# Optimization experiments

Measured on AMD Instinct MI355X. Metric: run time of the kernel, lower is better.

## Reference

```python
import jax, jax.numpy as jnp
import numpy as np

D_MODEL = 128
NUM_HEADS = 8
DEPTH = D_MODEL // NUM_HEADS
NEG = -1e9


def _dense_params(key, d_in, d_out):
    kw, kb = jax.random.split(key)
    # Glorot-uniform like keras Dense default
    lim = np.sqrt(6.0 / (d_in + d_out))
    w = jax.random.uniform(kw, (d_in, d_out), jnp.float32, -lim, lim)
    b = jnp.zeros((d_out,), jnp.float32)
    return w, b


def setup_inputs() -> dict:
    key = jax.random.key(0)
    ks = jax.random.split(key, 16)
    B, N, M, d = 256, 128, 128, D_MODEL
    inp = {
        'x_self': jax.random.normal(ks[0], (B, N, d), jnp.float32),
        'adj_self': jax.random.randint(ks[1], (B, N, N), 0, 2, jnp.int32),
        'mask_self': jnp.ones((B, N), jnp.int32),
        'x_cross': jax.random.normal(ks[2], (B, M, d), jnp.float32),
        'mask_cross': jnp.ones((B, M), jnp.int32),
    }
    names = ['wq_s', 'wk_s', 'wv_s', 'wo_s', 'wq_c', 'wk_c', 'wv_c', 'wo_c']
    for i, nm in enumerate(names):
        w, b = _dense_params(ks[3 + i], d, d)
        inp[nm] = w
        inp['b' + nm[1:]] = b
    wg, bg = _dense_params(ks[12], 3 * d, d)
    inp['wg'] = wg
    inp['bg'] = bg
    return inp


def _split_heads(x):
    B, N, _ = x.shape
    return x.reshape(B, N, NUM_HEADS, DEPTH).transpose(0, 2, 1, 3)  # [B,H,N,depth]


def _merge_heads(x):
    B, H, N, Dp = x.shape
    return x.transpose(0, 2, 1, 3).reshape(B, N, H * Dp)


def _attention(q, k, v, mask, adj=None):
    # q,k,v: [B,H,Nq,depth]; mask: [B,Nk]; adj: [B,Nq,Nk] or None
    logits = jnp.einsum('bhqd,bhkd->bhqk', q, k) / jnp.sqrt(jnp.float32(DEPTH))
    if adj is not None:
        logits = logits + ((1.0 - adj.astype(jnp.float32)) * NEG)[:, None, :, :]
    logits = logits + ((1.0 - mask.astype(jnp.float32)) * NEG)[:, None, None, :]
    w = jax.nn.softmax(logits, axis=-1)
    return jnp.einsum('bhqk,bhkd->bhqd', w, v)


def reference(x_self, adj_self, mask_self, x_cross, mask_cross,
              wq_s, bq_s, wk_s, bk_s, wv_s, bv_s, wo_s, bo_s,
              wq_c, bq_c, wk_c, bk_c, wv_c, bv_c, wo_c, bo_c,
              wg, bg):
    # Self attention (adjacency + padding mask)
    q_s = _split_heads(x_self @ wq_s + bq_s)
    k_s = _split_heads(x_self @ wk_s + bk_s)
    v_s = _split_heads(x_self @ wv_s + bv_s)
    out_s = _merge_heads(_attention(q_s, k_s, v_s, mask_self, adj_self)) @ wo_s + bo_s
    # Cross attention (padding mask only); dropout inactive at inference
    q_c = _split_heads(x_self @ wq_c + bq_c)
    k_c = _split_heads(x_cross @ wk_c + bk_c)
    v_c = _split_heads(x_cross @ wv_c + bv_c)
    out_c = _merge_heads(_attention(q_c, k_c, v_c, mask_cross)) @ wo_c + bo_c
    # Sigmoid gate fusion
    gate = jax.nn.sigmoid(jnp.concatenate([x_self, out_s, out_c], axis=-1) @ wg + bg)
    return (1.0 - gate) * out_s + gate * out_c
```

## Files before the change

### kernel.cpp

```cpp
#include <hip/hip_runtime.h>
#include <hip/hip_bf16.h>

typedef _Float16 f16_t;
typedef __attribute__((ext_vector_type(8))) _Float16 f16x8;
typedef __attribute__((ext_vector_type(4))) float f32x4;

#define LFENCE() asm volatile("" ::: "memory")

__device__ __forceinline__ f16x8 cvt8(const float* p) {
  float4 v0 = *(const float4*)p;
  float4 v1 = *(const float4*)(p + 4);
  f16x8 a;
  a[0] = (f16_t)v0.x; a[1] = (f16_t)v0.y; a[2] = (f16_t)v0.z; a[3] = (f16_t)v0.w;
  a[4] = (f16_t)v1.x; a[5] = (f16_t)v1.y; a[6] = (f16_t)v1.z; a[7] = (f16_t)v1.w;
  return a;
}

__global__ __launch_bounds__(256) void prep_kernel(
    const float* wq_s, const float* wk_s, const float* wv_s,
    const float* wq_c, const float* wk_c, const float* wv_c,
    const float* wo_s, const float* wo_c, const float* wg,
    const float* bos, const float* boc, const float* bgin,
    f16_t* WT, float* bgp)
{
  const int b = blockIdx.x;
  const int tid = threadIdx.x;
  if (b < 11) {
    __shared__ float t[128][129];
    const float* src; f16_t* dst; int ostride;
    switch (b) {
      case 0: src = wq_s; break; case 1: src = wk_s; break;
      case 2: src = wv_s; break; case 3: src = wq_c; break;
      case 4: src = wk_c; break; case 5: src = wv_c; break;
      case 6: src = wo_s; break; case 7: src = wo_c; break;
      default: src = wg + (size_t)(b - 8) * 16384; break;
    }
    if (b < 8) { dst = WT + (size_t)b * 16384; ostride = 128; }
    else       { dst = WT + 8 * 16384 + (b - 8) * 128; ostride = 384; }
#pragma unroll
    for (int i = 0; i < 64; ++i) {
      const int idx = tid + i * 256;
      t[idx & 127][idx >> 7] = src[idx];
    }
    __syncthreads();
#pragma unroll
    for (int i = 0; i < 64; ++i) {
      const int idx = tid + i * 256;
      const int c = idx >> 7, r = idx & 127;
      dst[(size_t)c * ostride + r] = (f16_t)t[c][r];
    }
  } else if (b < 13) {
    const int matsel = b - 11;
    const float* wo = matsel ? wo_c : wo_s;
    const int joff = 128 + matsel * 128;
    f16_t* dst = WT + (size_t)(11 + matsel) * 16384;
    const int wv = tid >> 6, ln = tid & 63, l15 = ln & 15, g = ln >> 4;
    f32x4 acc[2][8];
#pragma unroll
    for (int mm = 0; mm < 2; ++mm)
#pragma unroll
      for (int nt = 0; nt < 8; ++nt) acc[mm][nt] = (f32x4){0.f, 0.f, 0.f, 0.f};
#pragma unroll
    for (int kt = 0; kt < 4; ++kt) {
      f16x8 a[2];
#pragma unroll
      for (int mm = 0; mm < 2; ++mm) {
        const int crow = wv * 32 + mm * 16 + l15;
#pragma unroll
        for (int jj = 0; jj < 8; ++jj)
          a[mm][jj] = (f16_t)wg[(size_t)(joff + kt * 32 + g * 8 + jj) * 128 + crow];
      }
#pragma unroll
      for (int nt = 0; nt < 8; ++nt) {
        f16x8 bf = cvt8(wo + (size_t)(nt * 16 + l15) * 128 + kt * 32 + g * 8);
        acc[0][nt] = __builtin_amdgcn_mfma_f32_16x16x32_f16(a[0], bf, acc[0][nt], 0, 0, 0);
        acc[1][nt] = __builtin_amdgcn_mfma_f32_16x16x32_f16(a[1], bf, acc[1][nt], 0, 0, 0);
      }
    }
#pragma unroll
    for (int mm = 0; mm < 2; ++mm)
#pragma unroll
      for (int nt = 0; nt < 8; ++nt)
#pragma unroll
        for (int r = 0; r < 4; ++r) {
          const int c = wv * 32 + mm * 16 + g * 4 + r;
          dst[(size_t)c * 128 + nt * 16 + l15] = (f16_t)acc[mm][nt][r];
        }
  } else {
    if (tid < 128) {
      float acc = bgin[tid];
      for (int j = 0; j < 128; ++j)
        acc += bos[j] * wg[(size_t)(128 + j) * 128 + tid] +
               boc[j] * wg[(size_t)(256 + j) * 128 + tid];
      bgp[tid] = acc;
    }
  }
}

template <bool TRANSP>
__device__ __forceinline__ void gemm8(
    const f16x8 afr[4], const f16_t* __restrict__ W, const float* __restrict__ bias,
    char* Ob, int l15, int g, int rg)
{
  f32x4 acc[8];
#pragma unroll
  for (int nt = 0; nt < 8; ++nt) acc[nt] = (f32x4){0.f, 0.f, 0.f, 0.f};
#pragma unroll
  for (int nt = 0; nt < 8; ++nt)
#pragma unroll
    for (int kt = 0; kt < 4; ++kt) {
      f16x8 b = *(const f16x8*)(W + (size_t)(nt * 16 + l15) * 128 + kt * 32 + g * 8);
      acc[nt] = __builtin_amdgcn_mfma_f32_16x16x32_f16(afr[kt], b, acc[nt], 0, 0, 0);
    }
#pragma unroll
  for (int nt = 0; nt < 8; ++nt) {
    const int col = nt * 16 + l15;
    const float bv = bias[col];
#pragma unroll
    for (int r = 0; r < 4; ++r) {
      const int row = rg * 16 + g * 4 + r;
      const f16_t v = (f16_t)(acc[nt][r] + bv);
      if (TRANSP)
        *(f16_t*)(Ob + col * 256 + ((row * 2) ^ ((col & 7) << 4))) = v;
      else
        *(f16_t*)(Ob + row * 256 + ((col * 2) ^ ((row & 7) << 4))) = v;
    }
  }
}

__device__ __forceinline__ void gemmQ2(
    const f16x8 afr[4], const f16_t* __restrict__ W, const float* __restrict__ bias,
    char* scr, int l15, int g, f16x8 bq[8])
{
#pragma unroll
  for (int p = 0; p < 2; ++p) {
    LFENCE();
    f32x4 acc[4];
#pragma unroll
    for (int nt = 0; nt < 4; ++nt) acc[nt] = (f32x4){0.f, 0.f, 0.f, 0.f};
#pragma unroll
    for (int nt = 0; nt < 4; ++nt)
#pragma unroll
      for (int kt = 0; kt < 4; ++kt) {
        f16x8 b = *(const f16x8*)(W + (size_t)(p * 64 + nt * 16 + l15) * 128 + kt * 32 + g * 8);
        acc[nt] = __builtin_amdgcn_mfma_f32_16x16x32_f16(afr[kt], b, acc[nt], 0, 0, 0);
      }
#pragma unroll
    for (int nt = 0; nt < 4; ++nt) {
      const float bv = bias[p * 64 + nt * 16 + l15];
      const int dloc = nt * 16 + l15;
#pragma unroll
      for (int r = 0; r < 4; ++r) {
        const int qp = g * 4 + r;
        *(f16_t*)(scr + qp * 128 + ((dloc * 2) ^ ((qp & 7) << 4))) = (f16_t)(acc[nt][r] + bv);
      }
    }
    LFENCE();
#pragma unroll
    for (int h = 0; h < 4; ++h) {
      f16x8 z = {0, 0, 0, 0, 0, 0, 0, 0};
      bq[p * 4 + h] = (g < 2)
        ? *(const f16x8*)(scr + l15 * 128 + (((h * 16 + g * 8) * 2) ^ ((l15 & 7) << 4)))
        : z;
    }
  }
  LFENCE();
}

__global__ __launch_bounds__(512) void battn_kernel(
    const float* __restrict__ Xs, const float* __restrict__ Xc,
    const int* __restrict__ adj, const int* __restrict__ mask_s,
    const int* __restrict__ mask_c, const f16_t* __restrict__ WT,
    const float* __restrict__ bq_s, const float* __restrict__ bk_s,
    const float* __restrict__ bv_s, const float* __restrict__ bq_c,
    const float* __restrict__ bk_c, const float* __restrict__ bv_c,
    f16_t* __restrict__ att_s, f16_t* __restrict__ att_c)
{
  __shared__ __align__(16) char Kb[32768];
  __shared__ __align__(16) char Vtb[32768];
  __shared__ __align__(16) char WS[16384];

  const bool self = blockIdx.x < 256;
  const int bb = blockIdx.x & 255;
  const int tid = threadIdx.x;
  const int rg = tid >> 6, ln = tid & 63, l15 = ln & 15, g = ln >> 4;
  const int arow = rg * 16 + l15;
  char* scr = WS + rg * 2048;

  const f16_t* WQ = WT + (size_t)(self ? 0 : 3) * 16384;
  const f16_t* WK = WT + (size_t)(self ? 1 : 4) * 16384;
  const f16_t* WV = WT + (size_t)(self ? 2 : 5) * 16384;
  const float* bqv = self ? bq_s : bq_c;
  const float* bkv = self ? bk_s : bk_c;
  const float* bvv = self ? bv_s : bv_c;
  const float* XK  = self ? Xs : Xc;
  const int* mask  = self ? mask_s : mask_c;
  f16_t* ATT = self ? att_s : att_c;

  unsigned mw[4];
  {
    unsigned long long m0 = __ballot(mask[bb * 128 + ln] != 0);
    unsigned long long m1 = __ballot(mask[bb * 128 + 64 + ln] != 0);
    mw[0] = (unsigned)m0; mw[1] = (unsigned)(m0 >> 32);
    mw[2] = (unsigned)m1; mw[3] = (unsigned)(m1 >> 32);
  }
  unsigned aw[4];
  if (self) {
    const int row = rg * 16 + (ln & 15);
    const int w = ln >> 4;
    const int4* ap = (const int4*)(adj + ((size_t)bb * 128 + row) * 128 + w * 32);
    unsigned word = 0;
#pragma unroll
    for (int i = 0; i < 8; ++i) {
      int4 a = ap[i];
      word |= ((a.x != 0 ? 1u : 0u) | (a.y != 0 ? 2u : 0u) |
               (a.z != 0 ? 4u : 0u) | (a.w != 0 ? 8u : 0u)) << (i * 4);
    }
#pragma unroll
    for (int w2 = 0; w2 < 4; ++w2)
      aw[w2] = (unsigned)__shfl((int)word, w2 * 16 + l15) & mw[w2];
  } else {
#pragma unroll
    for (int w2 = 0; w2 < 4; ++w2) aw[w2] = mw[w2];
  }

  f16x8 bq[8];
  {
    f16x8 afrK[4];
#pragma unroll
    for (int kt = 0; kt < 4; ++kt)
      afrK[kt] = cvt8(XK + (size_t)bb * 16384 + arow * 128 + kt * 32 + g * 8);
    gemm8<false>(afrK, WK, bkv, Kb, l15, g, rg);
    gemm8<true >(afrK, WV, bvv, Vtb, l15, g, rg);
    f16x8 afrQ[4];
    if (self) {
#pragma unroll
      for (int kt = 0; kt < 4; ++kt) afrQ[kt] = afrK[kt];
    } else {
#pragma unroll
      for (int kt = 0; kt < 4; ++kt)
        afrQ[kt] = cvt8(Xs + (size_t)bb * 16384 + arow * 128 + kt * 32 + g * 8);
    }
    gemmQ2(afrQ, WQ, bqv, scr, l15, g, bq);
  }
  __syncthreads();

  const f32x4 zero = (f32x4){0.f, 0.f, 0.f, 0.f};
  char* Pw = scr;
#pragma unroll
  for (int h = 0; h < 8; ++h) {
    const int d = h * 16 + l15;
    float psum = 0.f;
    f32x4 o = zero;
#pragma unroll
    for (int c = 0; c < 4; ++c) {
      f32x4 st[2];
#pragma unroll
      for (int hf = 0; hf < 2; ++hf) {
        const int krow = (c * 2 + hf) * 16 + l15;
        f16x8 ak = {0, 0, 0, 0, 0, 0, 0, 0};
        if (g < 2)
          ak = *(const f16x8*)(Kb + krow * 256 + (((h * 16 + g * 8) * 2) ^ ((krow & 7) << 4)));
        st[hf] = __builtin_amdgcn_mfma_f32_16x16x32_f16(ak, bq[h], zero, 0, 0, 0);
      }
#pragma unroll
      for (int hf = 0; hf < 2; ++hf) {
        union { f16_t hh[4]; unsigned long long u; } pk;
#pragma unroll
        for (int r = 0; r < 4; ++r) {
          const int k = (c * 2 + hf) * 16 + g * 4 + r;
          const float e = __expf(st[hf][r] * 0.25f - 4.f);
          const float p = ((aw[k >> 5] >> (k & 31)) & 1u) ? e : 0.f;
          psum += p;
          pk.hh[r] = (f16_t)p;
        }
        *(unsigned long long*)(Pw + l15 * 80 + hf * 32 + g * 8) = pk.u;
      }
      LFENCE();
      union { unsigned long long u[2]; f16x8 v; } pa2;
      pa2.u[0] = *(const unsigned long long*)(Pw + l15 * 80 + g * 16);
      pa2.u[1] = *(const unsigned long long*)(Pw + l15 * 80 + g * 16 + 8);
      LFENCE();
      f16x8 vb = *(const f16x8*)(Vtb + d * 256 + (((c * 32 + g * 8) * 2) ^ ((d & 7) << 4)));
      o = __builtin_amdgcn_mfma_f32_16x16x32_f16(pa2.v, vb, o, 0, 0, 0);
    }
    psum += __shfl_xor(psum, 16);
    psum += __shfl_xor(psum, 32);
    const float inv = 1.f / psum;
#pragma unroll
    for (int r = 0; r < 4; ++r) {
      const float invq = __shfl(inv, g * 4 + r);
      const int row = rg * 16 + g * 4 + r;
      ATT[(size_t)bb * 16384 + row * 128 + h * 16 + l15] = (f16_t)(o[r] * invq);
    }
  }
}

__global__ __launch_bounds__(256) void outgate2_kernel(
    const f16_t* __restrict__ AS, const f16_t* __restrict__ AC,
    const float* __restrict__ X, const f16_t* __restrict__ WT,
    const float* __restrict__ bos, const float* __restrict__ boc,
    const float* __restrict__ bgp, float* __restrict__ OUT)
{
  const int tid = threadIdx.x;
  const int wv = tid >> 6, ln = tid & 63, l15 = ln & 15, g = ln >> 4;
  const int rowgrp = wv & 1, colgrp = wv >> 1;
  const size_t arow = (size_t)blockIdx.x * 32 + rowgrp * 16 + l15;
  const f16_t* WoS = WT + 6 * 16384;
  const f16_t* WoC = WT + 7 * 16384;
  const f16_t* WgT = WT + 8 * 16384;
  const f16_t* W2T = WT + 11 * 16384;
  const f16_t* W3T = WT + 12 * 16384;

  f32x4 accS[4], accC[4], accG[4];
#pragma unroll
  for (int nt = 0; nt < 4; ++nt) {
    accS[nt] = (f32x4){0.f, 0.f, 0.f, 0.f};
    accC[nt] = (f32x4){0.f, 0.f, 0.f, 0.f};
    accG[nt] = (f32x4){0.f, 0.f, 0.f, 0.f};
  }

#pragma unroll
  for (int kt = 0; kt < 4; ++kt) {
    const size_t ko = kt * 32 + g * 8;
    f16x8 aS = *(const f16x8*)(AS + arow * 128 + ko);
    f16x8 aC = *(const f16x8*)(AC + arow * 128 + ko);
    f16x8 aX = cvt8(X + arow * 128 + ko);
#pragma unroll
    for (int nt = 0; nt < 4; ++nt) {
      const size_t col = colgrp * 64 + nt * 16 + l15;
      f16x8 bS = *(const f16x8*)(WoS + col * 128 + ko);
      f16x8 bC = *(const f16x8*)(WoC + col * 128 + ko);
      f16x8 b2 = *(const f16x8*)(W2T + col * 128 + ko);
      f16x8 b3 = *(const f16x8*)(W3T + col * 128 + ko);
      f16x8 bX = *(const f16x8*)(WgT + col * 384 + ko);
      accS[nt] = __builtin_amdgcn_mfma_f32_16x16x32_f16(aS, bS, accS[nt], 0, 0, 0);
      accC[nt] = __builtin_amdgcn_mfma_f32_16x16x32_f16(aC, bC, accC[nt], 0, 0, 0);
      accG[nt] = __builtin_amdgcn_mfma_f32_16x16x32_f16(aX, bX, accG[nt], 0, 0, 0);
      accG[nt] = __builtin_amdgcn_mfma_f32_16x16x32_f16(aS, b2, accG[nt], 0, 0, 0);
      accG[nt] = __builtin_amdgcn_mfma_f32_16x16x32_f16(aC, b3, accG[nt], 0, 0, 0);
    }
  }

  const size_t orow0 = (size_t)blockIdx.x * 32 + rowgrp * 16 + g * 4;
#pragma unroll
  for (int nt = 0; nt < 4; ++nt) {
    const int col = colgrp * 64 + nt * 16 + l15;
    const float bS = bos[col], bC = boc[col], bG = bgp[col];
#pragma unroll
    for (int r = 0; r < 4; ++r) {
      const float os = accS[nt][r] + bS;
      const float oc = accC[nt][r] + bC;
      const float gv = 1.f / (1.f + __expf(-(accG[nt][r] + bG)));
      OUT[(orow0 + r) * 128 + col] = (1.f - gv) * os + gv * oc;
    }
  }
}

extern "C" void kernel_launch(void* const* d_in, const int* in_sizes, int n_in,
                              void* d_out, int out_size, void* d_ws, size_t ws_size,
                              hipStream_t stream)
{
  const float* x_self  = (const float*)d_in[0];
  const int*   adj     = (const int*)d_in[1];
  const int*   mask_s  = (const int*)d_in[2];
  const float* x_cross = (const float*)d_in[3];
  const int*   mask_c  = (const int*)d_in[4];
  const float* wq_s = (const float*)d_in[5];
  const float* bq_s = (const float*)d_in[6];
  const float* wk_s = (const float*)d_in[7];
  const float* bk_s = (const float*)d_in[8];
  const float* wv_s = (const float*)d_in[9];
  const float* bv_s = (const float*)d_in[10];
  const float* wo_s = (const float*)d_in[11];
  const float* bo_s = (const float*)d_in[12];
  const float* wq_c = (const float*)d_in[13];
  const float* bq_c = (const float*)d_in[14];
  const float* wk_c = (const float*)d_in[15];
  const float* bk_c = (const float*)d_in[16];
  const float* wv_c = (const float*)d_in[17];
  const float* bv_c = (const float*)d_in[18];
  const float* wo_c = (const float*)d_in[19];
  const float* bo_c = (const float*)d_in[20];
  const float* wg   = (const float*)d_in[21];
  const float* bg   = (const float*)d_in[22];
  float* out = (float*)d_out;

  const size_t SZ = (size_t)256 * 128 * 128;
  f16_t* WT  = (f16_t*)d_ws;
  float* bgp = (float*)(WT + 13 * 16384);
  f16_t* att_s = (f16_t*)(bgp + 128);
  f16_t* att_c = att_s + SZ;

  prep_kernel<<<14, 256, 0, stream>>>(wq_s, wk_s, wv_s, wq_c, wk_c, wv_c,
                                      wo_s, wo_c, wg, bo_s, bo_c, bg, WT, bgp);
  battn_kernel<<<512, 512, 0, stream>>>(x_self, x_cross, adj, mask_s, mask_c, WT,
                                        bq_s, bk_s, bv_s, bq_c, bk_c, bv_c,
                                        att_s, att_c);
  outgate2_kernel<<<1024, 256, 0, stream>>>(att_s, att_c, x_self, WT,
                                            bo_s, bo_c, bgp, out);
}
```

Baseline: 135.5 us.

## Split attention blocks by head group and halve outgate row tiles

The attention kernel now launches four blocks per (batch, self/cross) pair. Each block handles two heads (32 columns), so it computes only that slice of the K, V and Q projections, and its shared memory shrinks to about 28 KB with padded unswizzled K/Q rows. The output/gate kernel moves to 16-row blocks with each wave covering 32 columns, doubling its grid. The aim is more blocks and higher occupancy across the CUs. The cost is that X and the adjacency matrix are reloaded and converted four times, once per head group.

```diff
diff --git a/kernel.cpp b/kernel.cpp
--- a/kernel.cpp
+++ b/kernel.cpp
@@ -97,77 +97,7 @@
   }
 }
 
-template <bool TRANSP>
-__device__ __forceinline__ void gemm8(
-    const f16x8 afr[4], const f16_t* __restrict__ W, const float* __restrict__ bias,
-    char* Ob, int l15, int g, int rg)
-{
-  f32x4 acc[8];
-#pragma unroll
-  for (int nt = 0; nt < 8; ++nt) acc[nt] = (f32x4){0.f, 0.f, 0.f, 0.f};
-#pragma unroll
-  for (int nt = 0; nt < 8; ++nt)
-#pragma unroll
-    for (int kt = 0; kt < 4; ++kt) {
-      f16x8 b = *(const f16x8*)(W + (size_t)(nt * 16 + l15) * 128 + kt * 32 + g * 8);
-      acc[nt] = __builtin_amdgcn_mfma_f32_16x16x32_f16(afr[kt], b, acc[nt], 0, 0, 0);
-    }
-#pragma unroll
-  for (int nt = 0; nt < 8; ++nt) {
-    const int col = nt * 16 + l15;
-    const float bv = bias[col];
-#pragma unroll
-    for (int r = 0; r < 4; ++r) {
-      const int row = rg * 16 + g * 4 + r;
-      const f16_t v = (f16_t)(acc[nt][r] + bv);
-      if (TRANSP)
-        *(f16_t*)(Ob + col * 256 + ((row * 2) ^ ((col & 7) << 4))) = v;
-      else
-        *(f16_t*)(Ob + row * 256 + ((col * 2) ^ ((row & 7) << 4))) = v;
-    }
-  }
-}
-
-__device__ __forceinline__ void gemmQ2(
-    const f16x8 afr[4], const f16_t* __restrict__ W, const float* __restrict__ bias,
-    char* scr, int l15, int g, f16x8 bq[8])
-{
-#pragma unroll
-  for (int p = 0; p < 2; ++p) {
-    LFENCE();
-    f32x4 acc[4];
-#pragma unroll
-    for (int nt = 0; nt < 4; ++nt) acc[nt] = (f32x4){0.f, 0.f, 0.f, 0.f};
-#pragma unroll
-    for (int nt = 0; nt < 4; ++nt)
-#pragma unroll
-      for (int kt = 0; kt < 4; ++kt) {
-        f16x8 b = *(const f16x8*)(W + (size_t)(p * 64 + nt * 16 + l15) * 128 + kt * 32 + g * 8);
-        acc[nt] = __builtin_amdgcn_mfma_f32_16x16x32_f16(afr[kt], b, acc[nt], 0, 0, 0);
-      }
-#pragma unroll
-    for (int nt = 0; nt < 4; ++nt) {
-      const float bv = bias[p * 64 + nt * 16 + l15];
-      const int dloc = nt * 16 + l15;
-#pragma unroll
-      for (int r = 0; r < 4; ++r) {
-        const int qp = g * 4 + r;
-        *(f16_t*)(scr + qp * 128 + ((dloc * 2) ^ ((qp & 7) << 4))) = (f16_t)(acc[nt][r] + bv);
-      }
-    }
-    LFENCE();
-#pragma unroll
-    for (int h = 0; h < 4; ++h) {
-      f16x8 z = {0, 0, 0, 0, 0, 0, 0, 0};
-      bq[p * 4 + h] = (g < 2)
-        ? *(const f16x8*)(scr + l15 * 128 + (((h * 16 + g * 8) * 2) ^ ((l15 & 7) << 4)))
-        : z;
-    }
-  }
-  LFENCE();
-}
-
-__global__ __launch_bounds__(512) void battn_kernel(
+__global__ __launch_bounds__(512) void battn2_kernel(
     const float* __restrict__ Xs, const float* __restrict__ Xc,
     const int* __restrict__ adj, const int* __restrict__ mask_s,
     const int* __restrict__ mask_c, const f16_t* __restrict__ WT,
@@ -176,16 +106,19 @@
     const float* __restrict__ bk_c, const float* __restrict__ bv_c,
     f16_t* __restrict__ att_s, f16_t* __restrict__ att_c)
 {
-  __shared__ __align__(16) char Kb[32768];
-  __shared__ __align__(16) char Vtb[32768];
-  __shared__ __align__(16) char WS[16384];
-
-  const bool self = blockIdx.x < 256;
-  const int bb = blockIdx.x & 255;
+  __shared__ __align__(16) char Kb[128 * 80];
+  __shared__ __align__(16) char Vtb[32 * 256];
+  __shared__ __align__(16) char WS[8 * 1280];
+
+  const int bid = blockIdx.x;
+  const int bb = bid & 255;
+  const bool self = ((bid >> 8) & 1) == 0;
+  const int hg = bid >> 9;
+  const int colbase = hg * 32;
   const int tid = threadIdx.x;
   const int rg = tid >> 6, ln = tid & 63, l15 = ln & 15, g = ln >> 4;
   const int arow = rg * 16 + l15;
-  char* scr = WS + rg * 2048;
+  char* scr = WS + rg * 1280;
 
   const f16_t* WQ = WT + (size_t)(self ? 0 : 3) * 16384;
   const f16_t* WK = WT + (size_t)(self ? 1 : 4) * 16384;
@@ -224,32 +157,106 @@
     for (int w2 = 0; w2 < 4; ++w2) aw[w2] = mw[w2];
   }
 
-  f16x8 bq[8];
+  f16x8 bq[2];
   {
     f16x8 afrK[4];
 #pragma unroll
     for (int kt = 0; kt < 4; ++kt)
       afrK[kt] = cvt8(XK + (size_t)bb * 16384 + arow * 128 + kt * 32 + g * 8);
-    gemm8<false>(afrK, WK, bkv, Kb, l15, g, rg);
-    gemm8<true >(afrK, WV, bvv, Vtb, l15, g, rg);
-    f16x8 afrQ[4];
-    if (self) {
-#pragma unroll
-      for (int kt = 0; kt < 4; ++kt) afrQ[kt] = afrK[kt];
-    } else {
-#pragma unroll
-      for (int kt = 0; kt < 4; ++kt)
-        afrQ[kt] = cvt8(Xs + (size_t)bb * 16384 + arow * 128 + kt * 32 + g * 8);
-    }
-    gemmQ2(afrQ, WQ, bqv, scr, l15, g, bq);
+
+    {
+      f32x4 acc[2];
+      acc[0] = (f32x4){0.f, 0.f, 0.f, 0.f};
+      acc[1] = (f32x4){0.f, 0.f, 0.f, 0.f};
+#pragma unroll
+      for (int nt = 0; nt < 2; ++nt)
+#pragma unroll
+        for (int kt = 0; kt < 4; ++kt) {
+          f16x8 b = *(const f16x8*)(WK + (size_t)(colbase + nt * 16 + l15) * 128 + kt * 32 + g * 8);
+          acc[nt] = __builtin_amdgcn_mfma_f32_16x16x32_f16(afrK[kt], b, acc[nt], 0, 0, 0);
+        }
+#pragma unroll
+      for (int nt = 0; nt < 2; ++nt) {
+        const int lcol = nt * 16 + l15;
+        const float bv = bkv[colbase + lcol];
+#pragma unroll
+        for (int r = 0; r < 4; ++r) {
+          const int row = rg * 16 + g * 4 + r;
+          *(f16_t*)(Kb + row * 80 + lcol * 2) = (f16_t)(acc[nt][r] + bv);
+        }
+      }
+    }
+    {
+      f32x4 acc[2];
+      acc[0] = (f32x4){0.f, 0.f, 0.f, 0.f};
+      acc[1] = (f32x4){0.f, 0.f, 0.f, 0.f};
+#pragma unroll
+      for (int nt = 0; nt < 2; ++nt)
+#pragma unroll
+        for (int kt = 0; kt < 4; ++kt) {
+          f16x8 b = *(const f16x8*)(WV + (size_t)(colbase + nt * 16 + l15) * 128 + kt * 32 + g * 8);
+          acc[nt] = __builtin_amdgcn_mfma_f32_16x16x32_f16(afrK[kt], b, acc[nt], 0, 0, 0);
+        }
+#pragma unroll
+      for (int nt = 0; nt < 2; ++nt) {
+        const int lcol = nt * 16 + l15;
+        const float bv = bvv[colbase + lcol];
+#pragma unroll
+        for (int r = 0; r < 4; ++r) {
+          const int row = rg * 16 + g * 4 + r;
+          *(f16_t*)(Vtb + lcol * 256 + ((row * 2) ^ ((lcol & 7) << 4))) = (f16_t)(acc[nt][r] + bv);
+        }
+      }
+    }
+    {
+      f16x8 afrQ[4];
+      if (self) {
+#pragma unroll
+        for (int kt = 0; kt < 4; ++kt) afrQ[kt] = afrK[kt];
+      } else {
+#pragma unroll
+        for (int kt = 0; kt < 4; ++kt)
+          afrQ[kt] = cvt8(Xs + (size_t)bb * 16384 + arow * 128 + kt * 32 + g * 8);
+      }
+      LFENCE();
+      f32x4 acc[2];
+      acc[0] = (f32x4){0.f, 0.f, 0.f, 0.f};
+      acc[1] = (f32x4){0.f, 0.f, 0.f, 0.f};
+#pragma unroll
+      for (int nt = 0; nt < 2; ++nt)
+#pragma unroll
+        for (int kt = 0; kt < 4; ++kt) {
+          f16x8 b = *(const f16x8*)(WQ + (size_t)(colbase + nt * 16 + l15) * 128 + kt * 32 + g * 8);
+          acc[nt] = __builtin_amdgcn_mfma_f32_16x16x32_f16(afrQ[kt], b, acc[nt], 0, 0, 0);
+        }
+#pragma unroll
+      for (int nt = 0; nt < 2; ++nt) {
+        const int dloc = nt * 16 + l15;
+        const float bv = bqv[colbase + dloc];
+#pragma unroll
+        for (int r = 0; r < 4; ++r) {
+          const int qp = g * 4 + r;
+          *(f16_t*)(scr + qp * 80 + dloc * 2) = (f16_t)(acc[nt][r] + bv);
+        }
+      }
+      LFENCE();
+#pragma unroll
+      for (int h = 0; h < 2; ++h) {
+        f16x8 z = {0, 0, 0, 0, 0, 0, 0, 0};
+        bq[h] = (g < 2)
+          ? *(const f16x8*)(scr + l15 * 80 + (h * 16 + g * 8) * 2)
+          : z;
+      }
+      LFENCE();
+    }
   }
   __syncthreads();
 
   const f32x4 zero = (f32x4){0.f, 0.f, 0.f, 0.f};
   char* Pw = scr;
 #pragma unroll
-  for (int h = 0; h < 8; ++h) {
-    const int d = h * 16 + l15;
+  for (int h = 0; h < 2; ++h) {
+    const int dloc = h * 16 + l15;
     float psum = 0.f;
     f32x4 o = zero;
 #pragma unroll
@@ -260,7 +267,7 @@
         const int krow = (c * 2 + hf) * 16 + l15;
         f16x8 ak = {0, 0, 0, 0, 0, 0, 0, 0};
         if (g < 2)
-          ak = *(const f16x8*)(Kb + krow * 256 + (((h * 16 + g * 8) * 2) ^ ((krow & 7) << 4)));
+          ak = *(const f16x8*)(Kb + krow * 80 + (h * 16 + g * 8) * 2);
         st[hf] = __builtin_amdgcn_mfma_f32_16x16x32_f16(ak, bq[h], zero, 0, 0, 0);
       }
 #pragma unroll
@@ -281,7 +288,7 @@
       pa2.u[0] = *(const unsigned long long*)(Pw + l15 * 80 + g * 16);
       pa2.u[1] = *(const unsigned long long*)(Pw + l15 * 80 + g * 16 + 8);
       LFENCE();
-      f16x8 vb = *(const f16x8*)(Vtb + d * 256 + (((c * 32 + g * 8) * 2) ^ ((d & 7) << 4)));
+      f16x8 vb = *(const f16x8*)(Vtb + dloc * 256 + (((c * 32 + g * 8) * 2) ^ ((dloc & 7) << 4)));
       o = __builtin_amdgcn_mfma_f32_16x16x32_f16(pa2.v, vb, o, 0, 0, 0);
     }
     psum += __shfl_xor(psum, 16);
@@ -291,12 +298,12 @@
     for (int r = 0; r < 4; ++r) {
       const float invq = __shfl(inv, g * 4 + r);
       const int row = rg * 16 + g * 4 + r;
-      ATT[(size_t)bb * 16384 + row * 128 + h * 16 + l15] = (f16_t)(o[r] * invq);
+      ATT[(size_t)bb * 16384 + row * 128 + colbase + h * 16 + l15] = (f16_t)(o[r] * invq);
     }
   }
 }
 
-__global__ __launch_bounds__(256) void outgate2_kernel(
+__global__ __launch_bounds__(256) void outgate3_kernel(
     const f16_t* __restrict__ AS, const f16_t* __restrict__ AC,
     const float* __restrict__ X, const f16_t* __restrict__ WT,
     const float* __restrict__ bos, const float* __restrict__ boc,
@@ -304,17 +311,16 @@
 {
   const int tid = threadIdx.x;
   const int wv = tid >> 6, ln = tid & 63, l15 = ln & 15, g = ln >> 4;
-  const int rowgrp = wv & 1, colgrp = wv >> 1;
-  const size_t arow = (size_t)blockIdx.x * 32 + rowgrp * 16 + l15;
+  const size_t arow = (size_t)blockIdx.x * 16 + l15;
   const f16_t* WoS = WT + 6 * 16384;
   const f16_t* WoC = WT + 7 * 16384;
   const f16_t* WgT = WT + 8 * 16384;
   const f16_t* W2T = WT + 11 * 16384;
   const f16_t* W3T = WT + 12 * 16384;
 
-  f32x4 accS[4], accC[4], accG[4];
-#pragma unroll
-  for (int nt = 0; nt < 4; ++nt) {
+  f32x4 accS[2], accC[2], accG[2];
+#pragma unroll
+  for (int nt = 0; nt < 2; ++nt) {
     accS[nt] = (f32x4){0.f, 0.f, 0.f, 0.f};
     accC[nt] = (f32x4){0.f, 0.f, 0.f, 0.f};
     accG[nt] = (f32x4){0.f, 0.f, 0.f, 0.f};
@@ -327,8 +333,8 @@
     f16x8 aC = *(const f16x8*)(AC + arow * 128 + ko);
     f16x8 aX = cvt8(X + arow * 128 + ko);
 #pragma unroll
-    for (int nt = 0; nt < 4; ++nt) {
-      const size_t col = colgrp * 64 + nt * 16 + l15;
+    for (int nt = 0; nt < 2; ++nt) {
+      const size_t col = wv * 32 + nt * 16 + l15;
       f16x8 bS = *(const f16x8*)(WoS + col * 128 + ko);
       f16x8 bC = *(const f16x8*)(WoC + col * 128 + ko);
       f16x8 b2 = *(const f16x8*)(W2T + col * 128 + ko);
@@ -342,10 +348,10 @@
     }
   }
 
-  const size_t orow0 = (size_t)blockIdx.x * 32 + rowgrp * 16 + g * 4;
-#pragma unroll
-  for (int nt = 0; nt < 4; ++nt) {
-    const int col = colgrp * 64 + nt * 16 + l15;
+  const size_t orow0 = (size_t)blockIdx.x * 16 + g * 4;
+#pragma unroll
+  for (int nt = 0; nt < 2; ++nt) {
+    const int col = wv * 32 + nt * 16 + l15;
     const float bS = bos[col], bC = boc[col], bG = bgp[col];
 #pragma unroll
     for (int r = 0; r < 4; ++r) {
@@ -394,9 +400,9 @@
 
   prep_kernel<<<14, 256, 0, stream>>>(wq_s, wk_s, wv_s, wq_c, wk_c, wv_c,
                                       wo_s, wo_c, wg, bo_s, bo_c, bg, WT, bgp);
-  battn_kernel<<<512, 512, 0, stream>>>(x_self, x_cross, adj, mask_s, mask_c, WT,
-                                        bq_s, bk_s, bv_s, bq_c, bk_c, bv_c,
-                                        att_s, att_c);
-  outgate2_kernel<<<1024, 256, 0, stream>>>(att_s, att_c, x_self, WT,
+  battn2_kernel<<<2048, 512, 0, stream>>>(x_self, x_cross, adj, mask_s, mask_c, WT,
+                                          bq_s, bk_s, bv_s, bq_c, bk_c, bv_c,
+                                          att_s, att_c);
+  outgate3_kernel<<<2048, 256, 0, stream>>>(att_s, att_c, x_self, WT,
                                             bo_s, bo_c, bgp, out);
 }
```

Result: slower. 147.7 us (+9.0%).

## Fuse output projections and gate pre-activations into attention kernel, add blend pass

Applied to the files above, without the earlier changes.

The attention kernel now applies its own output projection (Wo) and its part of the gate logits. For self blocks that includes the x_self gate term, taken from the already-loaded X fragments. It stores the projected output as fp16 and the partial gate logits as fp32 per branch. A new elementwise blend kernel then sums the gate partials, applies the sigmoid and mixes the two branches. The aim is to stop re-reading x_self and to drop the separate output-GEMM kernel. In exchange the fp32 gate partials add intermediate write and read traffic, and the attention kernel carries more registers and a larger epilogue.

```diff
diff --git a/kernel.cpp b/kernel.cpp
--- a/kernel.cpp
+++ b/kernel.cpp
@@ -167,14 +167,17 @@
   LFENCE();
 }
 
-__global__ __launch_bounds__(512) void battn_kernel(
+__global__ __launch_bounds__(512) void battn4_kernel(
     const float* __restrict__ Xs, const float* __restrict__ Xc,
     const int* __restrict__ adj, const int* __restrict__ mask_s,
     const int* __restrict__ mask_c, const f16_t* __restrict__ WT,
     const float* __restrict__ bq_s, const float* __restrict__ bk_s,
     const float* __restrict__ bv_s, const float* __restrict__ bq_c,
     const float* __restrict__ bk_c, const float* __restrict__ bv_c,
-    f16_t* __restrict__ att_s, f16_t* __restrict__ att_c)
+    const float* __restrict__ bos, const float* __restrict__ boc,
+    const float* __restrict__ bgp,
+    f16_t* __restrict__ OS, f16_t* __restrict__ OC,
+    float* __restrict__ ZS, float* __restrict__ ZC)
 {
   __shared__ __align__(16) char Kb[32768];
   __shared__ __align__(16) char Vtb[32768];
@@ -190,12 +193,14 @@
   const f16_t* WQ = WT + (size_t)(self ? 0 : 3) * 16384;
   const f16_t* WK = WT + (size_t)(self ? 1 : 4) * 16384;
   const f16_t* WV = WT + (size_t)(self ? 2 : 5) * 16384;
+  const f16_t* WO = WT + (size_t)(self ? 6 : 7) * 16384;
+  const f16_t* WZ = WT + (size_t)(self ? 11 : 12) * 16384;
+  const f16_t* Wg1 = WT + 8 * 16384;
   const float* bqv = self ? bq_s : bq_c;
   const float* bkv = self ? bk_s : bk_c;
   const float* bvv = self ? bv_s : bv_c;
   const float* XK  = self ? Xs : Xc;
   const int* mask  = self ? mask_s : mask_c;
-  f16_t* ATT = self ? att_s : att_c;
 
   unsigned mw[4];
   {
@@ -225,8 +230,8 @@
   }
 
   f16x8 bq[8];
+  f16x8 afrK[4];
   {
-    f16x8 afrK[4];
 #pragma unroll
     for (int kt = 0; kt < 4; ++kt)
       afrK[kt] = cvt8(XK + (size_t)bb * 16384 + arow * 128 + kt * 32 + g * 8);
@@ -247,6 +252,7 @@
 
   const f32x4 zero = (f32x4){0.f, 0.f, 0.f, 0.f};
   char* Pw = scr;
+  f32x4 oall[8];
 #pragma unroll
   for (int h = 0; h < 8; ++h) {
     const int d = h * 16 + l15;
@@ -290,71 +296,85 @@
 #pragma unroll
     for (int r = 0; r < 4; ++r) {
       const float invq = __shfl(inv, g * 4 + r);
+      oall[h][r] = o[r] * invq;
+    }
+  }
+
+  f32x4 accO[8], accZ[8];
+#pragma unroll
+  for (int nt = 0; nt < 8; ++nt) { accO[nt] = zero; accZ[nt] = zero; }
+#pragma unroll
+  for (int kt = 0; kt < 4; ++kt) {
+    LFENCE();
+#pragma unroll
+    for (int hh2 = 0; hh2 < 2; ++hh2) {
+      const int h = kt * 2 + hh2;
+#pragma unroll
+      for (int r = 0; r < 4; ++r) {
+        const int rowl = g * 4 + r;
+        *(f16_t*)(scr + rowl * 80 + (hh2 * 16 + l15) * 2) = (f16_t)oall[h][r];
+      }
+    }
+    LFENCE();
+    f16x8 afrA = *(const f16x8*)(scr + l15 * 80 + g * 16);
+    LFENCE();
+    __builtin_amdgcn_s_setprio(1);
+#pragma unroll
+    for (int nt = 0; nt < 8; ++nt) {
+      const size_t col = nt * 16 + l15;
+      const size_t ko = kt * 32 + g * 8;
+      f16x8 bO = *(const f16x8*)(WO + col * 128 + ko);
+      f16x8 bZ = *(const f16x8*)(WZ + col * 128 + ko);
+      accO[nt] = __builtin_amdgcn_mfma_f32_16x16x32_f16(afrA, bO, accO[nt], 0, 0, 0);
+      accZ[nt] = __builtin_amdgcn_mfma_f32_16x16x32_f16(afrA, bZ, accZ[nt], 0, 0, 0);
+      if (self) {
+        f16x8 bG = *(const f16x8*)(Wg1 + col * 384 + ko);
+        accZ[nt] = __builtin_amdgcn_mfma_f32_16x16x32_f16(afrK[kt], bG, accZ[nt], 0, 0, 0);
+      }
+    }
+    __builtin_amdgcn_s_setprio(0);
+  }
+
+  const float* bo = self ? bos : boc;
+  f16_t* Ob = self ? OS : OC;
+  float* Zb = self ? ZS : ZC;
+#pragma unroll
+  for (int nt = 0; nt < 8; ++nt) {
+    const int col = nt * 16 + l15;
+    const float bv = bo[col];
+    const float bz = self ? bgp[col] : 0.f;
+#pragma unroll
+    for (int r = 0; r < 4; ++r) {
       const int row = rg * 16 + g * 4 + r;
-      ATT[(size_t)bb * 16384 + row * 128 + h * 16 + l15] = (f16_t)(o[r] * invq);
-    }
-  }
-}
-
-__global__ __launch_bounds__(256) void outgate2_kernel(
-    const f16_t* __restrict__ AS, const f16_t* __restrict__ AC,
-    const float* __restrict__ X, const f16_t* __restrict__ WT,
-    const float* __restrict__ bos, const float* __restrict__ boc,
-    const float* __restrict__ bgp, float* __restrict__ OUT)
-{
-  const int tid = threadIdx.x;
-  const int wv = tid >> 6, ln = tid & 63, l15 = ln & 15, g = ln >> 4;
-  const int rowgrp = wv & 1, colgrp = wv >> 1;
-  const size_t arow = (size_t)blockIdx.x * 32 + rowgrp * 16 + l15;
-  const f16_t* WoS = WT + 6 * 16384;
-  const f16_t* WoC = WT + 7 * 16384;
-  const f16_t* WgT = WT + 8 * 16384;
-  const f16_t* W2T = WT + 11 * 16384;
-  const f16_t* W3T = WT + 12 * 16384;
-
-  f32x4 accS[4], accC[4], accG[4];
-#pragma unroll
-  for (int nt = 0; nt < 4; ++nt) {
-    accS[nt] = (f32x4){0.f, 0.f, 0.f, 0.f};
-    accC[nt] = (f32x4){0.f, 0.f, 0.f, 0.f};
-    accG[nt] = (f32x4){0.f, 0.f, 0.f, 0.f};
-  }
-
-#pragma unroll
-  for (int kt = 0; kt < 4; ++kt) {
-    const size_t ko = kt * 32 + g * 8;
-    f16x8 aS = *(const f16x8*)(AS + arow * 128 + ko);
-    f16x8 aC = *(const f16x8*)(AC + arow * 128 + ko);
-    f16x8 aX = cvt8(X + arow * 128 + ko);
-#pragma unroll
-    for (int nt = 0; nt < 4; ++nt) {
-      const size_t col = colgrp * 64 + nt * 16 + l15;
-      f16x8 bS = *(const f16x8*)(WoS + col * 128 + ko);
-      f16x8 bC = *(const f16x8*)(WoC + col * 128 + ko);
-      f16x8 b2 = *(const f16x8*)(W2T + col * 128 + ko);
-      f16x8 b3 = *(const f16x8*)(W3T + col * 128 + ko);
-      f16x8 bX = *(const f16x8*)(WgT + col * 384 + ko);
-      accS[nt] = __builtin_amdgcn_mfma_f32_16x16x32_f16(aS, bS, accS[nt], 0, 0, 0);
-      accC[nt] = __builtin_amdgcn_mfma_f32_16x16x32_f16(aC, bC, accC[nt], 0, 0, 0);
-      accG[nt] = __builtin_amdgcn_mfma_f32_16x16x32_f16(aX, bX, accG[nt], 0, 0, 0);
-      accG[nt] = __builtin_amdgcn_mfma_f32_16x16x32_f16(aS, b2, accG[nt], 0, 0, 0);
-      accG[nt] = __builtin_amdgcn_mfma_f32_16x16x32_f16(aC, b3, accG[nt], 0, 0, 0);
-    }
-  }
-
-  const size_t orow0 = (size_t)blockIdx.x * 32 + rowgrp * 16 + g * 4;
-#pragma unroll
-  for (int nt = 0; nt < 4; ++nt) {
-    const int col = colgrp * 64 + nt * 16 + l15;
-    const float bS = bos[col], bC = boc[col], bG = bgp[col];
-#pragma unroll
-    for (int r = 0; r < 4; ++r) {
-      const float os = accS[nt][r] + bS;
-      const float oc = accC[nt][r] + bC;
-      const float gv = 1.f / (1.f + __expf(-(accG[nt][r] + bG)));
-      OUT[(orow0 + r) * 128 + col] = (1.f - gv) * os + gv * oc;
-    }
-  }
+      const size_t off = (size_t)bb * 16384 + row * 128 + col;
+      Ob[off] = (f16_t)(accO[nt][r] + bv);
+      Zb[off] = accZ[nt][r] + bz;
+    }
+  }
+}
+
+__global__ __launch_bounds__(256) void blend_kernel(
+    const f16_t* __restrict__ OS, const f16_t* __restrict__ OC,
+    const float* __restrict__ ZS, const float* __restrict__ ZC,
+    float* __restrict__ OUT)
+{
+  const size_t base = ((size_t)blockIdx.x * 256 + threadIdx.x) * 8;
+  f16x8 os = *(const f16x8*)(OS + base);
+  f16x8 oc = *(const f16x8*)(OC + base);
+  float4 zs0 = *(const float4*)(ZS + base);
+  float4 zs1 = *(const float4*)(ZS + base + 4);
+  float4 zc0 = *(const float4*)(ZC + base);
+  float4 zc1 = *(const float4*)(ZC + base + 4);
+  float z[8] = {zs0.x + zc0.x, zs0.y + zc0.y, zs0.z + zc0.z, zs0.w + zc0.w,
+                zs1.x + zc1.x, zs1.y + zc1.y, zs1.z + zc1.z, zs1.w + zc1.w};
+  float o[8];
+#pragma unroll
+  for (int j = 0; j < 8; ++j) {
+    const float gv = 1.f / (1.f + __expf(-z[j]));
+    o[j] = (1.f - gv) * (float)os[j] + gv * (float)oc[j];
+  }
+  *(float4*)(OUT + base) = (float4){o[0], o[1], o[2], o[3]};
+  *(float4*)(OUT + base + 4) = (float4){o[4], o[5], o[6], o[7]};
 }
 
 extern "C" void kernel_launch(void* const* d_in, const int* in_sizes, int n_in,
@@ -389,14 +409,15 @@
   const size_t SZ = (size_t)256 * 128 * 128;
   f16_t* WT  = (f16_t*)d_ws;
   float* bgp = (float*)(WT + 13 * 16384);
-  f16_t* att_s = (f16_t*)(bgp + 128);
-  f16_t* att_c = att_s + SZ;
+  f16_t* OS = (f16_t*)(bgp + 128);
+  f16_t* OC = OS + SZ;
+  float* ZS = (float*)(OC + SZ);
+  float* ZC = ZS + SZ;
 
   prep_kernel<<<14, 256, 0, stream>>>(wq_s, wk_s, wv_s, wq_c, wk_c, wv_c,
                                       wo_s, wo_c, wg, bo_s, bo_c, bg, WT, bgp);
-  battn_kernel<<<512, 512, 0, stream>>>(x_self, x_cross, adj, mask_s, mask_c, WT,
-                                        bq_s, bk_s, bv_s, bq_c, bk_c, bv_c,
-                                        att_s, att_c);
-  outgate2_kernel<<<1024, 256, 0, stream>>>(att_s, att_c, x_self, WT,
-                                            bo_s, bo_c, bgp, out);
-}
+  battn4_kernel<<<512, 512, 0, stream>>>(x_self, x_cross, adj, mask_s, mask_c, WT,
+                                         bq_s, bk_s, bv_s, bq_c, bk_c, bv_c,
+                                         bo_s, bo_c, bgp, OS, OC, ZS, ZC);
+  blend_kernel<<<2048, 256, 0, stream>>>(OS, OC, ZS, ZC, out);
+}
```

New measurement: 139.9 us. +3.2%, slower.
